# Optimization experiments

Hardware: AMD Instinct MI355X
Metric: run time of the kernel (lower is better)

Reference implementation:

```python
import jax, jax.numpy as jnp
import numpy as np

N_F, N_C = 100000, 25000          # fine / coarse node counts
C_IN, C_OUT = 128, 128
E_POOL, E = 200000, 400000        # pooling edges, coarse point-point edges


def setup_inputs() -> dict:
    key = jax.random.key(0)
    ks = jax.random.split(key, 12)
    x = jax.random.normal(ks[0], (N_F, C_IN), jnp.float32)
    # pooling edges: src in fine graph, dst in coarse graph
    pool_src = jax.random.randint(ks[1], (E_POOL,), 0, N_F, dtype=jnp.int64)
    pool_dst = jax.random.randint(ks[2], (E_POOL,), 0, N_C, dtype=jnp.int64)
    pool_edge_index = jnp.stack([pool_src, pool_dst])
    pool_edge_attr = jax.random.uniform(ks[3], (E_POOL,), jnp.float32)
    # coarse point-point edges
    src = jax.random.randint(ks[4], (E,), 0, N_C, dtype=jnp.int64)
    dst = jax.random.randint(ks[5], (E,), 0, N_C, dtype=jnp.int64)
    edge_index = jnp.stack([src, dst])
    edge_attr = jax.random.uniform(ks[6], (E,), jnp.float32)
    s_in = 1.0 / np.sqrt(C_IN).astype(np.float32)
    s_out = 1.0 / np.sqrt(C_OUT).astype(np.float32)
    W1_root = jax.random.normal(ks[7], (C_IN, C_OUT), jnp.float32) * s_in
    W1_nb = jax.random.normal(ks[8], (C_IN, C_OUT), jnp.float32) * s_in
    b1 = jnp.zeros((C_OUT,), jnp.float32)
    W2_root = jax.random.normal(ks[9], (C_OUT, C_OUT), jnp.float32) * s_out
    W2_nb = jax.random.normal(ks[10], (C_OUT, C_OUT), jnp.float32) * s_out
    b2 = jnp.zeros((C_OUT,), jnp.float32)
    return {
        "x": x,
        "pool_edge_index": pool_edge_index,
        "pool_edge_attr": pool_edge_attr,
        "edge_index": edge_index,
        "edge_attr": edge_attr,
        "W1_root": W1_root, "W1_nb": W1_nb, "b1": b1,
        "W2_root": W2_root, "W2_nb": W2_nb, "b2": b2,
        "n_coarse": N_C,
    }


def _graph_conv(h, edge_index, edge_attr, W_root, W_nb, b, n_nodes):
    # GraphConv with edge weights: out = h @ W_root + scatter_add(w_e * (h[src] @ W_nb), dst) + b
    msg = edge_attr[:, None] * (h[edge_index[0]] @ W_nb)          # [E, C_out]
    agg = jax.ops.segment_sum(msg, edge_index[1], num_segments=n_nodes)
    return h @ W_root + agg + b


def reference(x, pool_edge_index, pool_edge_attr, edge_index, edge_attr,
              W1_root, W1_nb, b1, W2_root, W2_nb, b2, n_coarse):
    # CustomPoolingAdd: weighted scatter-add fine -> coarse
    pooled = jax.ops.segment_sum(pool_edge_attr[:, None] * x[pool_edge_index[0]],
                                 pool_edge_index[1], num_segments=n_coarse)  # [N_c, C_in]
    h = _graph_conv(pooled, edge_index, edge_attr, W1_root, W1_nb, b1, n_coarse)
    h = _graph_conv(h, edge_index, edge_attr, W2_root, W2_nb, b2, n_coarse)
    return h
```

## Files before the change

### kernel.cpp

```cpp
#include <hip/hip_runtime.h>

typedef __attribute__((ext_vector_type(8))) short   short8;
typedef __attribute__((ext_vector_type(8))) __bf16  bf16x8;
typedef __attribute__((ext_vector_type(4))) float   f32x4;

__device__ __forceinline__ float bf2f(unsigned short u) {
    union { unsigned int i; float f; } v; v.i = ((unsigned int)u) << 16; return v.f;
}
__device__ __forceinline__ unsigned short f2bf(float f) {
    union { float f; unsigned int i; } v; v.f = f;
    unsigned int r = v.i + 0x7fffu + ((v.i >> 16) & 1u);
    return (unsigned short)(r >> 16);
}

__device__ __forceinline__ int load_idx(const void* p, int is64, long long i) {
    return is64 ? (int)((const long long*)p)[i] : ((const int*)p)[i];
}
__device__ __forceinline__ float load_f(const void* p, int isbf, long long i) {
    return isbf ? bf2f(((const unsigned short*)p)[i]) : ((const float*)p)[i];
}

__device__ __forceinline__ int self_is64(const int* p) {
    int lane = threadIdx.x & 63;
    unsigned long long b = __ballot(p[2 * lane + 1] != 0);
    return b == 0ull;
}
__device__ __forceinline__ int self_isbf(const unsigned int* p) {
    int lane = threadIdx.x & 63;
    unsigned int lo = p[lane] & 0xFFFFu;
    int e = (int)((lo >> 7) & 0xFF);
    int ok = (lo == 0u) || (e >= 88 && e <= 141);
    return (__ballot(!ok) == 0ull) ? 1 : 0;
}

__global__ void detect_kernel(const int* __restrict__ pei, const int* __restrict__ ei,
                              const unsigned int* f0, const unsigned int* f1,
                              const unsigned int* f2, const unsigned int* f3,
                              const unsigned int* f4, const unsigned int* f5,
                              const unsigned int* f6, const unsigned int* f7,
                              const unsigned int* f8,
                              int* __restrict__ flags) {
    int lane = threadIdx.x & 63;
    unsigned long long ba = __ballot(pei[2 * lane + 1] != 0);
    unsigned long long bb = __ballot(ei[2 * lane + 1] != 0);
    const unsigned int* fa[9] = {f0, f1, f2, f3, f4, f5, f6, f7, f8};
    int bf[9];
    #pragma unroll
    for (int t = 0; t < 9; t++) {
        unsigned int lo = fa[t][lane] & 0xFFFFu;
        int e = (int)((lo >> 7) & 0xFF);
        int ok = (lo == 0u) || (e >= 88 && e <= 141);
        bf[t] = (__ballot(!ok) == 0ull) ? 1 : 0;
    }
    if (lane == 0) {
        flags[0] = (ba == 0ull);
        flags[1] = (bb == 0ull);
        #pragma unroll
        for (int t = 0; t < 9; t++) flags[2 + t] = bf[t];
    }
}

#define BKT_CAP 64
#define OVF_CAP 4096
#define CNT_STRIDE 16

__global__ void fillpack_kernel(const void* __restrict__ pei, const void* __restrict__ pattr,
                                const void* __restrict__ ei, const void* __restrict__ eattr,
                                int* __restrict__ pcnt, int2* __restrict__ pbkt,
                                int* __restrict__ povfc, int4* __restrict__ povf,
                                int* __restrict__ ccnt, int2* __restrict__ cbkt,
                                int* __restrict__ covfc, int4* __restrict__ covf,
                                int Ep, int Ec, int gE,
                                const void* __restrict__ w1r, const void* __restrict__ w1n,
                                const void* __restrict__ w2r, const void* __restrict__ w2n,
                                unsigned short* __restrict__ wpack) {
    if ((int)blockIdx.x >= gE) {
        int gid = ((int)blockIdx.x - gE) * 256 + threadIdx.x;
        int layer = gid >> 15;
        int r = gid & 32767;
        int j = r & 7, lane = (r >> 3) & 63, ch = (r >> 9) & 7, ct = (r >> 12) & 7;
        int n = ct * 16 + (lane & 15);
        int k = ch * 32 + (lane >> 4) * 8 + j;
        const void* w;
        if (layer == 0) w = (k < 128) ? w1r : w1n;
        else            w = (k < 128) ? w2r : w2n;
        int fs = self_isbf((const unsigned int*)w);
        float v = load_f(w, fs, (long long)(k & 127) * 128 + n);
        wpack[gid] = f2bf(v);
        return;
    }
    long long g = (long long)blockIdx.x * 256 + threadIdx.x;
    if (g < Ep) {
        int is64 = self_is64((const int*)pei);
        int abf = self_isbf((const unsigned int*)pattr);
        int s = load_idx(pei, is64, g);
        int d = load_idx(pei, is64, (long long)Ep + g);
        float w = load_f(pattr, abf, g);
        int pos = atomicAdd(&pcnt[d * CNT_STRIDE], 1);
        if (pos < BKT_CAP) {
            pbkt[(long long)d * BKT_CAP + pos] = make_int2(s, __float_as_int(w));
        } else {
            int oi = atomicAdd(povfc, 1);
            if (oi < OVF_CAP) povf[oi] = make_int4(s, __float_as_int(w), d, 0);
        }
    } else if (g - Ep < Ec) {
        long long e = g - Ep;
        int is64 = self_is64((const int*)ei);
        int abf = self_isbf((const unsigned int*)eattr);
        int s = load_idx(ei, is64, e);
        int d = load_idx(ei, is64, (long long)Ec + e);
        float w = load_f(eattr, abf, e);
        int pos = atomicAdd(&ccnt[d * CNT_STRIDE], 1);
        if (pos < BKT_CAP) {
            cbkt[(long long)d * BKT_CAP + pos] = make_int2(s, __float_as_int(w));
        } else {
            int oi = atomicAdd(covfc, 1);
            if (oi < OVF_CAP) covf[oi] = make_int4(s, __float_as_int(w), d, 0);
        }
    }
}

__global__ void gatherb_kernel(const void* __restrict__ in,
                               const int* __restrict__ cnt,
                               const int2* __restrict__ bkt,
                               const int* __restrict__ ovfc,
                               const int4* __restrict__ ovf,
                               unsigned short* __restrict__ out, int NC,
                               int detectIn) {
    int d = blockIdx.x * 4 + (threadIdx.x >> 6);
    if (d >= NC) return;
    int lane = threadIdx.x & 63;
    int j1 = cnt[d * CNT_STRIDE]; if (j1 > BKT_CAP) j1 = BKT_CAP;
    const int2* row = bkt + (long long)d * BKT_CAP;
    float ax = 0.f, ay = 0.f;
    int bf = detectIn ? self_isbf((const unsigned int*)in) : 1;
    if (!bf) {
        const float* fin = (const float*)in;
        int c0 = lane * 2;
        int j = 0;
        for (; j + 8 <= j1; j += 8) {
            int2 e0 = row[j], e1 = row[j + 1], e2 = row[j + 2], e3 = row[j + 3];
            int2 e4 = row[j + 4], e5 = row[j + 5], e6 = row[j + 6], e7 = row[j + 7];
            float2 v0 = *(const float2*)(fin + (long long)e0.x * 128 + c0);
            float2 v1 = *(const float2*)(fin + (long long)e1.x * 128 + c0);
            float2 v2 = *(const float2*)(fin + (long long)e2.x * 128 + c0);
            float2 v3 = *(const float2*)(fin + (long long)e3.x * 128 + c0);
            float2 v4 = *(const float2*)(fin + (long long)e4.x * 128 + c0);
            float2 v5 = *(const float2*)(fin + (long long)e5.x * 128 + c0);
            float2 v6 = *(const float2*)(fin + (long long)e6.x * 128 + c0);
            float2 v7 = *(const float2*)(fin + (long long)e7.x * 128 + c0);
            ax += __int_as_float(e0.y) * v0.x + __int_as_float(e1.y) * v1.x
                + __int_as_float(e2.y) * v2.x + __int_as_float(e3.y) * v3.x
                + __int_as_float(e4.y) * v4.x + __int_as_float(e5.y) * v5.x
                + __int_as_float(e6.y) * v6.x + __int_as_float(e7.y) * v7.x;
            ay += __int_as_float(e0.y) * v0.y + __int_as_float(e1.y) * v1.y
                + __int_as_float(e2.y) * v2.y + __int_as_float(e3.y) * v3.y
                + __int_as_float(e4.y) * v4.y + __int_as_float(e5.y) * v5.y
                + __int_as_float(e6.y) * v6.y + __int_as_float(e7.y) * v7.y;
        }
        for (; j + 4 <= j1; j += 4) {
            int2 e0 = row[j], e1 = row[j + 1], e2 = row[j + 2], e3 = row[j + 3];
            float2 v0 = *(const float2*)(fin + (long long)e0.x * 128 + c0);
            float2 v1 = *(const float2*)(fin + (long long)e1.x * 128 + c0);
            float2 v2 = *(const float2*)(fin + (long long)e2.x * 128 + c0);
            float2 v3 = *(const float2*)(fin + (long long)e3.x * 128 + c0);
            ax += __int_as_float(e0.y) * v0.x + __int_as_float(e1.y) * v1.x
                + __int_as_float(e2.y) * v2.x + __int_as_float(e3.y) * v3.x;
            ay += __int_as_float(e0.y) * v0.y + __int_as_float(e1.y) * v1.y
                + __int_as_float(e2.y) * v2.y + __int_as_float(e3.y) * v3.y;
        }
        for (; j < j1; j++) {
            int2 e = row[j];
            float w = __int_as_float(e.y);
            float2 v = *(const float2*)(fin + (long long)e.x * 128 + c0);
            ax += w * v.x; ay += w * v.y;
        }
        int novf = *ovfc;
        if (novf > 0) {
            if (novf > OVF_CAP) novf = OVF_CAP;
            for (int k = 0; k < novf; k++) {
                int4 e = ovf[k];
                if (e.z == d) {
                    float w = __int_as_float(e.y);
                    float2 v = *(const float2*)(fin + (long long)e.x * 128 + c0);
                    ax += w * v.x; ay += w * v.y;
                }
            }
        }
    } else {
        const unsigned int* uin = (const unsigned int*)in;
        int j = 0;
        for (; j + 8 <= j1; j += 8) {
            int2 e0 = row[j], e1 = row[j + 1], e2 = row[j + 2], e3 = row[j + 3];
            int2 e4 = row[j + 4], e5 = row[j + 5], e6 = row[j + 6], e7 = row[j + 7];
            unsigned int v0 = uin[(long long)e0.x * 64 + lane];
            unsigned int v1 = uin[(long long)e1.x * 64 + lane];
            unsigned int v2 = uin[(long long)e2.x * 64 + lane];
            unsigned int v3 = uin[(long long)e3.x * 64 + lane];
            unsigned int v4 = uin[(long long)e4.x * 64 + lane];
            unsigned int v5 = uin[(long long)e5.x * 64 + lane];
            unsigned int v6 = uin[(long long)e6.x * 64 + lane];
            unsigned int v7 = uin[(long long)e7.x * 64 + lane];
            ax += __int_as_float(e0.y) * bf2f((unsigned short)v0)
                + __int_as_float(e1.y) * bf2f((unsigned short)v1)
                + __int_as_float(e2.y) * bf2f((unsigned short)v2)
                + __int_as_float(e3.y) * bf2f((unsigned short)v3)
                + __int_as_float(e4.y) * bf2f((unsigned short)v4)
                + __int_as_float(e5.y) * bf2f((unsigned short)v5)
                + __int_as_float(e6.y) * bf2f((unsigned short)v6)
                + __int_as_float(e7.y) * bf2f((unsigned short)v7);
            ay += __int_as_float(e0.y) * bf2f((unsigned short)(v0 >> 16))
                + __int_as_float(e1.y) * bf2f((unsigned short)(v1 >> 16))
                + __int_as_float(e2.y) * bf2f((unsigned short)(v2 >> 16))
                + __int_as_float(e3.y) * bf2f((unsigned short)(v3 >> 16))
                + __int_as_float(e4.y) * bf2f((unsigned short)(v4 >> 16))
                + __int_as_float(e5.y) * bf2f((unsigned short)(v5 >> 16))
                + __int_as_float(e6.y) * bf2f((unsigned short)(v6 >> 16))
                + __int_as_float(e7.y) * bf2f((unsigned short)(v7 >> 16));
        }
        for (; j + 4 <= j1; j += 4) {
            int2 e0 = row[j], e1 = row[j + 1], e2 = row[j + 2], e3 = row[j + 3];
            unsigned int v0 = uin[(long long)e0.x * 64 + lane];
            unsigned int v1 = uin[(long long)e1.x * 64 + lane];
            unsigned int v2 = uin[(long long)e2.x * 64 + lane];
            unsigned int v3 = uin[(long long)e3.x * 64 + lane];
            ax += __int_as_float(e0.y) * bf2f((unsigned short)v0)
                + __int_as_float(e1.y) * bf2f((unsigned short)v1)
                + __int_as_float(e2.y) * bf2f((unsigned short)v2)
                + __int_as_float(e3.y) * bf2f((unsigned short)v3);
            ay += __int_as_float(e0.y) * bf2f((unsigned short)(v0 >> 16))
                + __int_as_float(e1.y) * bf2f((unsigned short)(v1 >> 16))
                + __int_as_float(e2.y) * bf2f((unsigned short)(v2 >> 16))
                + __int_as_float(e3.y) * bf2f((unsigned short)(v3 >> 16));
        }
        for (; j < j1; j++) {
            int2 e = row[j];
            float w = __int_as_float(e.y);
            unsigned int v = uin[(long long)e.x * 64 + lane];
            ax += w * bf2f((unsigned short)v);
            ay += w * bf2f((unsigned short)(v >> 16));
        }
        int novf = *ovfc;
        if (novf > 0) {
            if (novf > OVF_CAP) novf = OVF_CAP;
            for (int k = 0; k < novf; k++) {
                int4 e = ovf[k];
                if (e.z == d) {
                    float w = __int_as_float(e.y);
                    unsigned int v = uin[(long long)e.x * 64 + lane];
                    ax += w * bf2f((unsigned short)v);
                    ay += w * bf2f((unsigned short)(v >> 16));
                }
            }
        }
    }
    unsigned int o = (unsigned int)f2bf(ax) | ((unsigned int)f2bf(ay) << 16);
    ((unsigned int*)out)[(long long)d * 64 + lane] = o;
}

__global__ __launch_bounds__(256, 4)
void gemm_mfma_kernel(const unsigned short* __restrict__ H,
                      const unsigned short* __restrict__ G,
                      const unsigned short* __restrict__ wpack,
                      const void* __restrict__ bias,
                      float* __restrict__ outF, unsigned short* __restrict__ outB,
                      int NC) {
    __shared__ unsigned short ldsA[64 * 264];
    int tid = threadIdx.x;
    long long r0 = (long long)blockIdx.x * 64;
    for (int i = tid; i < 4096; i += 256) {
        int mat = i >> 11;
        int flat = i & 2047;
        int row = flat >> 5;
        int c4 = flat & 31;
        long long r = r0 + row;
        const unsigned short* srcp = mat ? G : H;
        uint2 v = make_uint2(0u, 0u);
        if (r < NC) v = *(const uint2*)(srcp + r * 128 + c4 * 4);
        *(uint2*)&ldsA[row * 264 + mat * 128 + c4 * 4] = v;
    }
    __syncthreads();

    int wave = tid >> 6, lane = tid & 63;
    int m = lane & 15, quad = lane >> 4;
    int arow = wave * 16 + m;

    bf16x8 a[8];
    #pragma unroll
    for (int ch = 0; ch < 8; ch++) {
        short8 av = *(const short8*)&ldsA[arow * 264 + ch * 32 + quad * 8];
        a[ch] = __builtin_bit_cast(bf16x8, av);
    }

    f32x4 acc[8];
    #pragma unroll
    for (int ct = 0; ct < 8; ct++) acc[ct] = (f32x4){0.f, 0.f, 0.f, 0.f};

    #pragma unroll
    for (int ct = 0; ct < 8; ct++) {
        #pragma unroll
        for (int ch = 0; ch < 8; ch++) {
            short8 bv = *(const short8*)(wpack + ((ct * 8 + ch) * 64 + lane) * 8);
            acc[ct] = __builtin_amdgcn_mfma_f32_16x16x32_bf16(
                a[ch], __builtin_bit_cast(bf16x8, bv), acc[ct], 0, 0, 0);
        }
    }

    int bbf = self_isbf((const unsigned int*)bias);
    #pragma unroll
    for (int ct = 0; ct < 8; ct++) {
        int n = ct * 16 + m;
        float bv = load_f(bias, bbf, n);
        #pragma unroll
        for (int r = 0; r < 4; r++) {
            long long rr = r0 + wave * 16 + quad * 4 + r;
            if (rr < NC) {
                float val = acc[ct][r] + bv;
                if (outF) outF[rr * 128 + n] = val;
                else      outB[rr * 128 + n] = f2bf(val);
            }
        }
    }
}

__global__ void pool_scatter_kernel(const void* __restrict__ x, const void* __restrict__ pei,
                                    const void* __restrict__ pattr, const int* __restrict__ flags,
                                    float* __restrict__ pooled, int Ep, int CI) {
    int c = blockIdx.y * blockDim.x + threadIdx.x;
    if (c >= CI) return;
    int e = blockIdx.x;
    int is64 = flags[0], xbf = flags[2], abf = flags[3];
    int s = load_idx(pei, is64, e);
    int d = load_idx(pei, is64, (long long)Ep + e);
    float w = load_f(pattr, abf, e);
    float v = load_f(x, xbf, (long long)s * CI + c);
    atomicAdd(&pooled[(long long)d * CI + c], w * v);
}

__global__ void conv_scatter_kernel(const float* __restrict__ t, const void* __restrict__ ei,
                                    const void* __restrict__ attr, const int* __restrict__ flags,
                                    float* __restrict__ outacc, int Ec, int CO) {
    int c = blockIdx.y * blockDim.x + threadIdx.x;
    if (c >= CO) return;
    int e = blockIdx.x;
    int is64 = flags[1], abf = flags[4];
    int s = load_idx(ei, is64, e);
    int d = load_idx(ei, is64, (long long)Ec + e);
    float w = load_f(attr, abf, e);
    atomicAdd(&outacc[(long long)d * CO + c], w * t[(long long)s * CO + c]);
}

__global__ void gemm_kernel(const float* H, const void* __restrict__ Wr,
                            const void* __restrict__ Wn, const void* __restrict__ bias,
                            const int* __restrict__ flags, int fWr, int fWn, int fB,
                            float* out_root, float* out_t, int NC, int CI, int CO) {
    __shared__ float lds[4][1024];
    int wave = threadIdx.x >> 6;
    int lane = threadIdx.x & 63;
    int r = blockIdx.x * 4 + wave;
    if (r < NC) {
        const float* hrow = H + (long long)r * CI;
        for (int k = lane; k < CI; k += 64) lds[wave][k] = hrow[k];
    }
    __syncthreads();
    if (r >= NC) return;
    int wrbf = flags[fWr], wnbf = flags[fWn], bbf = flags[fB];
    for (int c0 = lane * 2; c0 < CO; c0 += 128) {
        int two = (c0 + 1 < CO);
        float ar0 = 0.f, ar1 = 0.f, an0 = 0.f, an1 = 0.f;
        for (int k = 0; k < CI; k++) {
            float h = lds[wave][k];
            ar0 += h * load_f(Wr, wrbf, (long long)k * CO + c0);
            an0 += h * load_f(Wn, wnbf, (long long)k * CO + c0);
            if (two) {
                ar1 += h * load_f(Wr, wrbf, (long long)k * CO + c0 + 1);
                an1 += h * load_f(Wn, wnbf, (long long)k * CO + c0 + 1);
            }
        }
        long long o = (long long)r * CO + c0;
        out_root[o] = ar0 + load_f(bias, bbf, c0);
        out_t[o] = an0;
        if (two) {
            out_root[o + 1] = ar1 + load_f(bias, bbf, c0 + 1);
            out_t[o + 1] = an1;
        }
    }
}

__global__ void to_out_kernel(const float* __restrict__ in, float* __restrict__ out, long long n) {
    long long stride = (long long)gridDim.x * blockDim.x;
    for (long long i = (long long)blockIdx.x * blockDim.x + threadIdx.x; i < n; i += stride)
        out[i] = in[i];
}

extern "C" void kernel_launch(void* const* d_in, const int* in_sizes, int n_in,
                              void* d_out, int out_size, void* d_ws, size_t ws_size,
                              hipStream_t stream) {
    const void* x = d_in[0]; const void* pei = d_in[1]; const void* pattr = d_in[2];
    const void* ei = d_in[3]; const void* eattr = d_in[4];
    const void* w1r = d_in[5]; const void* w1n = d_in[6]; const void* b1 = d_in[7];
    const void* w2r = d_in[8]; const void* w2n = d_in[9]; const void* b2 = d_in[10];

    long long CO = in_sizes[7];
    long long CI = CO > 0 ? in_sizes[5] / CO : 0;
    long long Ep = in_sizes[2];
    long long Ec = in_sizes[4];
    long long NC = CO > 0 ? (long long)out_size / CO : 0;
    int sane = (CO > 0 && CI > 0 && CI <= 1024 && CO <= 1024 &&
                CI * CO == in_sizes[5] && NC * CO == out_size &&
                Ep > 0 && Ec > 0 && in_sizes[0] % CI == 0);
    if (!sane) { CO = 128; CI = 128; Ep = 200000; Ec = 400000; NC = 25000; }

    char* ws = (char*)d_ws;

    if (CI == 128 && CO == 128) {
        size_t off = 0;
        unsigned short* bufP = (unsigned short*)(ws + off); off += (size_t)NC * 128 * 2;
        unsigned short* bufH = (unsigned short*)(ws + off); off += (size_t)NC * 128 * 2;
        unsigned short* bufG = (unsigned short*)(ws + off); off += (size_t)NC * 128 * 2;
        unsigned short* wpack = (unsigned short*)(ws + off); off += 65536 * 2;
        int* pcnt  = (int*)(ws + off); off += NC * CNT_STRIDE * 4;
        int* ccnt  = (int*)(ws + off); off += NC * CNT_STRIDE * 4;
        int* povfc = (int*)(ws + off); off += 4;
        int* covfc = (int*)(ws + off); off += 4;
        off = (off + 15) & ~(size_t)15;
        int4* povf = (int4*)(ws + off); off += (size_t)OVF_CAP * 16;
        int4* covf = (int4*)(ws + off); off += (size_t)OVF_CAP * 16;
        int2* pbkt = (int2*)(ws + off); off += (size_t)NC * BKT_CAP * 8;
        int2* cbkt = (int2*)(ws + off); off += (size_t)NC * BKT_CAP * 8;

        hipMemsetAsync(pcnt, 0, (2 * NC * CNT_STRIDE + 2) * 4, stream);

        int gE = (int)((Ep + Ec + 255) / 256);
        fillpack_kernel<<<gE + 256, 256, 0, stream>>>(pei, pattr, ei, eattr,
                                                      pcnt, pbkt, povfc, povf,
                                                      ccnt, cbkt, covfc, covf,
                                                      (int)Ep, (int)Ec, gE,
                                                      w1r, w1n, w2r, w2n, wpack);

        int gN4 = (int)((NC + 3) / 4);
        int gN64 = (int)((NC + 63) / 64);
        gatherb_kernel<<<gN4, 256, 0, stream>>>(x, pcnt, pbkt, povfc, povf, bufP, (int)NC, 1);
        gatherb_kernel<<<gN4, 256, 0, stream>>>(bufP, ccnt, cbkt, covfc, covf, bufG, (int)NC, 0);
        gemm_mfma_kernel<<<gN64, 256, 0, stream>>>(bufP, bufG, wpack, b1,
                                                   nullptr, bufH, (int)NC);
        gatherb_kernel<<<gN4, 256, 0, stream>>>(bufH, ccnt, cbkt, covfc, covf, bufG, (int)NC, 0);
        gemm_mfma_kernel<<<gN64, 256, 0, stream>>>(bufH, bufG, wpack + 32768, b2,
                                                   (float*)d_out, nullptr, (int)NC);
        return;
    }

    size_t szP = (size_t)NC * CI * sizeof(float);
    size_t szO = (size_t)NC * CO * sizeof(float);
    float *bufP, *bufA, *bufB, *bufC; int* flags;
    if (CI == CO) {
        bufP = (float*)ws; bufA = (float*)(ws + szP);
        bufB = bufP; bufC = bufA;
        flags = (int*)(ws + szP + szO);
    } else {
        bufP = (float*)ws; bufA = (float*)(ws + szP);
        bufB = (float*)(ws + szP + szO); bufC = (float*)(ws + szP + 2 * szO);
        flags = (int*)(ws + szP + 3 * szO);
    }
    detect_kernel<<<1, 64, 0, stream>>>(
        (const int*)pei, (const int*)ei,
        (const unsigned int*)x, (const unsigned int*)pattr, (const unsigned int*)eattr,
        (const unsigned int*)w1r, (const unsigned int*)w1n, (const unsigned int*)b1,
        (const unsigned int*)w2r, (const unsigned int*)w2n, (const unsigned int*)b2,
        flags);
    hipMemsetAsync(bufP, 0, szP, stream);
    int blkP = (CI % 64 == 0 && CI <= 256) ? (int)CI : 256;
    int blkC = (CO % 64 == 0 && CO <= 256) ? (int)CO : 256;
    dim3 gP((unsigned)Ep, (unsigned)((CI + blkP - 1) / blkP));
    dim3 gC((unsigned)Ec, (unsigned)((CO + blkC - 1) / blkC));
    int gG = (int)((NC + 3) / 4);
    pool_scatter_kernel<<<gP, blkP, 0, stream>>>(x, pei, pattr, flags, bufP, (int)Ep, (int)CI);
    if (CI == CO) {
        gemm_kernel<<<gG, 256, 0, stream>>>(bufP, w1r, w1n, b1, flags, 5, 6, 7,
                                            bufA, bufP, (int)NC, (int)CI, (int)CO);
        conv_scatter_kernel<<<gC, blkC, 0, stream>>>(bufP, ei, eattr, flags, bufA, (int)Ec, (int)CO);
        gemm_kernel<<<gG, 256, 0, stream>>>(bufA, w2r, w2n, b2, flags, 8, 9, 10,
                                            bufP, bufA, (int)NC, (int)CO, (int)CO);
        conv_scatter_kernel<<<gC, blkC, 0, stream>>>(bufA, ei, eattr, flags, bufP, (int)Ec, (int)CO);
        to_out_kernel<<<4096, 256, 0, stream>>>(bufP, (float*)d_out, NC * CO);
    } else {
        gemm_kernel<<<gG, 256, 0, stream>>>(bufP, w1r, w1n, b1, flags, 5, 6, 7,
                                            bufA, bufB, (int)NC, (int)CI, (int)CO);
        conv_scatter_kernel<<<gC, blkC, 0, stream>>>(bufB, ei, eattr, flags, bufA, (int)Ec, (int)CO);
        gemm_kernel<<<gG, 256, 0, stream>>>(bufA, w2r, w2n, b2, flags, 8, 9, 10,
                                            bufB, bufC, (int)NC, (int)CO, (int)CO);
        conv_scatter_kernel<<<gC, blkC, 0, stream>>>(bufC, ei, eattr, flags, bufB, (int)Ec, (int)CO);
        to_out_kernel<<<4096, 256, 0, stream>>>(bufB, (float*)d_out, NC * CO);
    }
}
```

Measured before the change: 235.0 us.

## Pre-convert fine features to bf16 and compact bucket counters

Adds extra blocks to the edge-bucketing kernel that convert the fp32 fine-node features x into a bf16 copy in workspace, when the workspace is large enough. The pooling gather then reads half as many bytes per random row through a new gatherx kernel. Per-node counters are packed densely instead of padded to 16 ints, which shrinks the memset, and the pooling bucket capacity drops to 32. The trade-off is an extra streaming pass over x, extra rounding of the input features to bf16, and possibly more atomic contention on the densely packed counters.

```diff
diff --git a/kernel.cpp b/kernel.cpp
--- a/kernel.cpp
+++ b/kernel.cpp
@@ -60,9 +60,9 @@
     }
 }
 
-#define BKT_CAP 64
+#define PBKT_CAP 32
+#define CBKT_CAP 64
 #define OVF_CAP 4096
-#define CNT_STRIDE 16
 
 __global__ void fillpack_kernel(const void* __restrict__ pei, const void* __restrict__ pattr,
                                 const void* __restrict__ ei, const void* __restrict__ eattr,
@@ -73,9 +73,35 @@
                                 int Ep, int Ec, int gE,
                                 const void* __restrict__ w1r, const void* __restrict__ w1n,
                                 const void* __restrict__ w2r, const void* __restrict__ w2n,
-                                unsigned short* __restrict__ wpack) {
-    if ((int)blockIdx.x >= gE) {
-        int gid = ((int)blockIdx.x - gE) * 256 + threadIdx.x;
+                                unsigned short* __restrict__ wpack,
+                                const void* __restrict__ x, unsigned short* __restrict__ xb,
+                                long long elemsX) {
+    int bid = (int)blockIdx.x;
+    if (bid >= gE + 256) {
+        int xisbf = self_isbf((const unsigned int*)x);
+        if (xisbf) return;
+        long long gid = (long long)(bid - gE - 256) * 256 + threadIdx.x;
+        long long row = gid >> 3;
+        int part = (int)(gid & 7);
+        long long NF = elemsX >> 7;
+        if (row >= NF) return;
+        const float4* src = (const float4*)((const float*)x + row * 128 + part * 16);
+        float4 a = src[0], b = src[1], c = src[2], d = src[3];
+        uint4 o0, o1;
+        o0.x = (unsigned int)f2bf(a.x) | ((unsigned int)f2bf(a.y) << 16);
+        o0.y = (unsigned int)f2bf(a.z) | ((unsigned int)f2bf(a.w) << 16);
+        o0.z = (unsigned int)f2bf(b.x) | ((unsigned int)f2bf(b.y) << 16);
+        o0.w = (unsigned int)f2bf(b.z) | ((unsigned int)f2bf(b.w) << 16);
+        o1.x = (unsigned int)f2bf(c.x) | ((unsigned int)f2bf(c.y) << 16);
+        o1.y = (unsigned int)f2bf(c.z) | ((unsigned int)f2bf(c.w) << 16);
+        o1.z = (unsigned int)f2bf(d.x) | ((unsigned int)f2bf(d.y) << 16);
+        o1.w = (unsigned int)f2bf(d.z) | ((unsigned int)f2bf(d.w) << 16);
+        uint4* dst = (uint4*)(xb + row * 128 + part * 16);
+        dst[0] = o0; dst[1] = o1;
+        return;
+    }
+    if (bid >= gE) {
+        int gid = (bid - gE) * 256 + threadIdx.x;
         int layer = gid >> 15;
         int r = gid & 32767;
         int j = r & 7, lane = (r >> 3) & 63, ch = (r >> 9) & 7, ct = (r >> 12) & 7;
@@ -89,16 +115,16 @@
         wpack[gid] = f2bf(v);
         return;
     }
-    long long g = (long long)blockIdx.x * 256 + threadIdx.x;
+    long long g = (long long)bid * 256 + threadIdx.x;
     if (g < Ep) {
         int is64 = self_is64((const int*)pei);
         int abf = self_isbf((const unsigned int*)pattr);
         int s = load_idx(pei, is64, g);
         int d = load_idx(pei, is64, (long long)Ep + g);
         float w = load_f(pattr, abf, g);
-        int pos = atomicAdd(&pcnt[d * CNT_STRIDE], 1);
-        if (pos < BKT_CAP) {
-            pbkt[(long long)d * BKT_CAP + pos] = make_int2(s, __float_as_int(w));
+        int pos = atomicAdd(&pcnt[d], 1);
+        if (pos < PBKT_CAP) {
+            pbkt[(long long)d * PBKT_CAP + pos] = make_int2(s, __float_as_int(w));
         } else {
             int oi = atomicAdd(povfc, 1);
             if (oi < OVF_CAP) povf[oi] = make_int4(s, __float_as_int(w), d, 0);
@@ -110,9 +136,9 @@
         int s = load_idx(ei, is64, e);
         int d = load_idx(ei, is64, (long long)Ec + e);
         float w = load_f(eattr, abf, e);
-        int pos = atomicAdd(&ccnt[d * CNT_STRIDE], 1);
-        if (pos < BKT_CAP) {
-            cbkt[(long long)d * BKT_CAP + pos] = make_int2(s, __float_as_int(w));
+        int pos = atomicAdd(&ccnt[d], 1);
+        if (pos < CBKT_CAP) {
+            cbkt[(long long)d * CBKT_CAP + pos] = make_int2(s, __float_as_int(w));
         } else {
             int oi = atomicAdd(covfc, 1);
             if (oi < OVF_CAP) covf[oi] = make_int4(s, __float_as_int(w), d, 0);
@@ -120,104 +146,23 @@
     }
 }
 
-__global__ void gatherb_kernel(const void* __restrict__ in,
+__global__ void gatherx_kernel(const void* __restrict__ x,
+                               const unsigned short* __restrict__ xb, int haveXb,
                                const int* __restrict__ cnt,
                                const int2* __restrict__ bkt,
                                const int* __restrict__ ovfc,
                                const int4* __restrict__ ovf,
-                               unsigned short* __restrict__ out, int NC,
-                               int detectIn) {
+                               unsigned short* __restrict__ out, int NC) {
     int d = blockIdx.x * 4 + (threadIdx.x >> 6);
     if (d >= NC) return;
     int lane = threadIdx.x & 63;
-    int j1 = cnt[d * CNT_STRIDE]; if (j1 > BKT_CAP) j1 = BKT_CAP;
-    const int2* row = bkt + (long long)d * BKT_CAP;
+    int j1 = cnt[d]; if (j1 > PBKT_CAP) j1 = PBKT_CAP;
+    const int2* row = bkt + (long long)d * PBKT_CAP;
     float ax = 0.f, ay = 0.f;
-    int bf = detectIn ? self_isbf((const unsigned int*)in) : 1;
-    if (!bf) {
-        const float* fin = (const float*)in;
-        int c0 = lane * 2;
+    int xisbf = self_isbf((const unsigned int*)x);
+    if (xisbf || haveXb) {
+        const unsigned int* uin = xisbf ? (const unsigned int*)x : (const unsigned int*)xb;
         int j = 0;
-        for (; j + 8 <= j1; j += 8) {
-            int2 e0 = row[j], e1 = row[j + 1], e2 = row[j + 2], e3 = row[j + 3];
-            int2 e4 = row[j + 4], e5 = row[j + 5], e6 = row[j + 6], e7 = row[j + 7];
-            float2 v0 = *(const float2*)(fin + (long long)e0.x * 128 + c0);
-            float2 v1 = *(const float2*)(fin + (long long)e1.x * 128 + c0);
-            float2 v2 = *(const float2*)(fin + (long long)e2.x * 128 + c0);
-            float2 v3 = *(const float2*)(fin + (long long)e3.x * 128 + c0);
-            float2 v4 = *(const float2*)(fin + (long long)e4.x * 128 + c0);
-            float2 v5 = *(const float2*)(fin + (long long)e5.x * 128 + c0);
-            float2 v6 = *(const float2*)(fin + (long long)e6.x * 128 + c0);
-            float2 v7 = *(const float2*)(fin + (long long)e7.x * 128 + c0);
-            ax += __int_as_float(e0.y) * v0.x + __int_as_float(e1.y) * v1.x
-                + __int_as_float(e2.y) * v2.x + __int_as_float(e3.y) * v3.x
-                + __int_as_float(e4.y) * v4.x + __int_as_float(e5.y) * v5.x
-                + __int_as_float(e6.y) * v6.x + __int_as_float(e7.y) * v7.x;
-            ay += __int_as_float(e0.y) * v0.y + __int_as_float(e1.y) * v1.y
-                + __int_as_float(e2.y) * v2.y + __int_as_float(e3.y) * v3.y
-                + __int_as_float(e4.y) * v4.y + __int_as_float(e5.y) * v5.y
-                + __int_as_float(e6.y) * v6.y + __int_as_float(e7.y) * v7.y;
-        }
-        for (; j + 4 <= j1; j += 4) {
-            int2 e0 = row[j], e1 = row[j + 1], e2 = row[j + 2], e3 = row[j + 3];
-            float2 v0 = *(const float2*)(fin + (long long)e0.x * 128 + c0);
-            float2 v1 = *(const float2*)(fin + (long long)e1.x * 128 + c0);
-            float2 v2 = *(const float2*)(fin + (long long)e2.x * 128 + c0);
-            float2 v3 = *(const float2*)(fin + (long long)e3.x * 128 + c0);
-            ax += __int_as_float(e0.y) * v0.x + __int_as_float(e1.y) * v1.x
-                + __int_as_float(e2.y) * v2.x + __int_as_float(e3.y) * v3.x;
-            ay += __int_as_float(e0.y) * v0.y + __int_as_float(e1.y) * v1.y
-                + __int_as_float(e2.y) * v2.y + __int_as_float(e3.y) * v3.y;
-        }
-        for (; j < j1; j++) {
-            int2 e = row[j];
-            float w = __int_as_float(e.y);
-            float2 v = *(const float2*)(fin + (long long)e.x * 128 + c0);
-            ax += w * v.x; ay += w * v.y;
-        }
-        int novf = *ovfc;
-        if (novf > 0) {
-            if (novf > OVF_CAP) novf = OVF_CAP;
-            for (int k = 0; k < novf; k++) {
-                int4 e = ovf[k];
-                if (e.z == d) {
-                    float w = __int_as_float(e.y);
-                    float2 v = *(const float2*)(fin + (long long)e.x * 128 + c0);
-                    ax += w * v.x; ay += w * v.y;
-                }
-            }
-        }
-    } else {
-        const unsigned int* uin = (const unsigned int*)in;
-        int j = 0;
-        for (; j + 8 <= j1; j += 8) {
-            int2 e0 = row[j], e1 = row[j + 1], e2 = row[j + 2], e3 = row[j + 3];
-            int2 e4 = row[j + 4], e5 = row[j + 5], e6 = row[j + 6], e7 = row[j + 7];
-            unsigned int v0 = uin[(long long)e0.x * 64 + lane];
-            unsigned int v1 = uin[(long long)e1.x * 64 + lane];
-            unsigned int v2 = uin[(long long)e2.x * 64 + lane];
-            unsigned int v3 = uin[(long long)e3.x * 64 + lane];
-            unsigned int v4 = uin[(long long)e4.x * 64 + lane];
-            unsigned int v5 = uin[(long long)e5.x * 64 + lane];
-            unsigned int v6 = uin[(long long)e6.x * 64 + lane];
-            unsigned int v7 = uin[(long long)e7.x * 64 + lane];
-            ax += __int_as_float(e0.y) * bf2f((unsigned short)v0)
-                + __int_as_float(e1.y) * bf2f((unsigned short)v1)
-                + __int_as_float(e2.y) * bf2f((unsigned short)v2)
-                + __int_as_float(e3.y) * bf2f((unsigned short)v3)
-                + __int_as_float(e4.y) * bf2f((unsigned short)v4)
-                + __int_as_float(e5.y) * bf2f((unsigned short)v5)
-                + __int_as_float(e6.y) * bf2f((unsigned short)v6)
-                + __int_as_float(e7.y) * bf2f((unsigned short)v7);
-            ay += __int_as_float(e0.y) * bf2f((unsigned short)(v0 >> 16))
-                + __int_as_float(e1.y) * bf2f((unsigned short)(v1 >> 16))
-                + __int_as_float(e2.y) * bf2f((unsigned short)(v2 >> 16))
-                + __int_as_float(e3.y) * bf2f((unsigned short)(v3 >> 16))
-                + __int_as_float(e4.y) * bf2f((unsigned short)(v4 >> 16))
-                + __int_as_float(e5.y) * bf2f((unsigned short)(v5 >> 16))
-                + __int_as_float(e6.y) * bf2f((unsigned short)(v6 >> 16))
-                + __int_as_float(e7.y) * bf2f((unsigned short)(v7 >> 16));
-        }
         for (; j + 4 <= j1; j += 4) {
             int2 e0 = row[j], e1 = row[j + 1], e2 = row[j + 2], e3 = row[j + 3];
             unsigned int v0 = uin[(long long)e0.x * 64 + lane];
@@ -251,6 +196,120 @@
                     ax += w * bf2f((unsigned short)v);
                     ay += w * bf2f((unsigned short)(v >> 16));
                 }
+            }
+        }
+    } else {
+        const float* fin = (const float*)x;
+        int c0 = lane * 2;
+        int j = 0;
+        for (; j + 4 <= j1; j += 4) {
+            int2 e0 = row[j], e1 = row[j + 1], e2 = row[j + 2], e3 = row[j + 3];
+            float2 v0 = *(const float2*)(fin + (long long)e0.x * 128 + c0);
+            float2 v1 = *(const float2*)(fin + (long long)e1.x * 128 + c0);
+            float2 v2 = *(const float2*)(fin + (long long)e2.x * 128 + c0);
+            float2 v3 = *(const float2*)(fin + (long long)e3.x * 128 + c0);
+            ax += __int_as_float(e0.y) * v0.x + __int_as_float(e1.y) * v1.x
+                + __int_as_float(e2.y) * v2.x + __int_as_float(e3.y) * v3.x;
+            ay += __int_as_float(e0.y) * v0.y + __int_as_float(e1.y) * v1.y
+                + __int_as_float(e2.y) * v2.y + __int_as_float(e3.y) * v3.y;
+        }
+        for (; j < j1; j++) {
+            int2 e = row[j];
+            float w = __int_as_float(e.y);
+            float2 v = *(const float2*)(fin + (long long)e.x * 128 + c0);
+            ax += w * v.x; ay += w * v.y;
+        }
+        int novf = *ovfc;
+        if (novf > 0) {
+            if (novf > OVF_CAP) novf = OVF_CAP;
+            for (int k = 0; k < novf; k++) {
+                int4 e = ovf[k];
+                if (e.z == d) {
+                    float w = __int_as_float(e.y);
+                    float2 v = *(const float2*)(fin + (long long)e.x * 128 + c0);
+                    ax += w * v.x; ay += w * v.y;
+                }
+            }
+        }
+    }
+    unsigned int o = (unsigned int)f2bf(ax) | ((unsigned int)f2bf(ay) << 16);
+    ((unsigned int*)out)[(long long)d * 64 + lane] = o;
+}
+
+__global__ void gatherb_kernel(const unsigned short* __restrict__ in,
+                               const int* __restrict__ cnt,
+                               const int2* __restrict__ bkt, int cap,
+                               const int* __restrict__ ovfc,
+                               const int4* __restrict__ ovf,
+                               unsigned short* __restrict__ out, int NC) {
+    int d = blockIdx.x * 4 + (threadIdx.x >> 6);
+    if (d >= NC) return;
+    int lane = threadIdx.x & 63;
+    int j1 = cnt[d]; if (j1 > cap) j1 = cap;
+    const int2* row = bkt + (long long)d * cap;
+    float ax = 0.f, ay = 0.f;
+    const unsigned int* uin = (const unsigned int*)in;
+    int j = 0;
+    for (; j + 8 <= j1; j += 8) {
+        int2 e0 = row[j], e1 = row[j + 1], e2 = row[j + 2], e3 = row[j + 3];
+        int2 e4 = row[j + 4], e5 = row[j + 5], e6 = row[j + 6], e7 = row[j + 7];
+        unsigned int v0 = uin[(long long)e0.x * 64 + lane];
+        unsigned int v1 = uin[(long long)e1.x * 64 + lane];
+        unsigned int v2 = uin[(long long)e2.x * 64 + lane];
+        unsigned int v3 = uin[(long long)e3.x * 64 + lane];
+        unsigned int v4 = uin[(long long)e4.x * 64 + lane];
+        unsigned int v5 = uin[(long long)e5.x * 64 + lane];
+        unsigned int v6 = uin[(long long)e6.x * 64 + lane];
+        unsigned int v7 = uin[(long long)e7.x * 64 + lane];
+        ax += __int_as_float(e0.y) * bf2f((unsigned short)v0)
+            + __int_as_float(e1.y) * bf2f((unsigned short)v1)
+            + __int_as_float(e2.y) * bf2f((unsigned short)v2)
+            + __int_as_float(e3.y) * bf2f((unsigned short)v3)
+            + __int_as_float(e4.y) * bf2f((unsigned short)v4)
+            + __int_as_float(e5.y) * bf2f((unsigned short)v5)
+            + __int_as_float(e6.y) * bf2f((unsigned short)v6)
+            + __int_as_float(e7.y) * bf2f((unsigned short)v7);
+        ay += __int_as_float(e0.y) * bf2f((unsigned short)(v0 >> 16))
+            + __int_as_float(e1.y) * bf2f((unsigned short)(v1 >> 16))
+            + __int_as_float(e2.y) * bf2f((unsigned short)(v2 >> 16))
+            + __int_as_float(e3.y) * bf2f((unsigned short)(v3 >> 16))
+            + __int_as_float(e4.y) * bf2f((unsigned short)(v4 >> 16))
+            + __int_as_float(e5.y) * bf2f((unsigned short)(v5 >> 16))
+            + __int_as_float(e6.y) * bf2f((unsigned short)(v6 >> 16))
+            + __int_as_float(e7.y) * bf2f((unsigned short)(v7 >> 16));
+    }
+    for (; j + 4 <= j1; j += 4) {
+        int2 e0 = row[j], e1 = row[j + 1], e2 = row[j + 2], e3 = row[j + 3];
+        unsigned int v0 = uin[(long long)e0.x * 64 + lane];
+        unsigned int v1 = uin[(long long)e1.x * 64 + lane];
+        unsigned int v2 = uin[(long long)e2.x * 64 + lane];
+        unsigned int v3 = uin[(long long)e3.x * 64 + lane];
+        ax += __int_as_float(e0.y) * bf2f((unsigned short)v0)
+            + __int_as_float(e1.y) * bf2f((unsigned short)v1)
+            + __int_as_float(e2.y) * bf2f((unsigned short)v2)
+            + __int_as_float(e3.y) * bf2f((unsigned short)v3);
+        ay += __int_as_float(e0.y) * bf2f((unsigned short)(v0 >> 16))
+            + __int_as_float(e1.y) * bf2f((unsigned short)(v1 >> 16))
+            + __int_as_float(e2.y) * bf2f((unsigned short)(v2 >> 16))
+            + __int_as_float(e3.y) * bf2f((unsigned short)(v3 >> 16));
+    }
+    for (; j < j1; j++) {
+        int2 e = row[j];
+        float w = __int_as_float(e.y);
+        unsigned int v = uin[(long long)e.x * 64 + lane];
+        ax += w * bf2f((unsigned short)v);
+        ay += w * bf2f((unsigned short)(v >> 16));
+    }
+    int novf = *ovfc;
+    if (novf > 0) {
+        if (novf > OVF_CAP) novf = OVF_CAP;
+        for (int k = 0; k < novf; k++) {
+            int4 e = ovf[k];
+            if (e.z == d) {
+                float w = __int_as_float(e.y);
+                unsigned int v = uin[(long long)e.x * 64 + lane];
+                ax += w * bf2f((unsigned short)v);
+                ay += w * bf2f((unsigned short)(v >> 16));
             }
         }
     }
@@ -414,37 +473,48 @@
     char* ws = (char*)d_ws;
 
     if (CI == 128 && CO == 128) {
+        long long elemsX = in_sizes[0];
         size_t off = 0;
         unsigned short* bufP = (unsigned short*)(ws + off); off += (size_t)NC * 128 * 2;
         unsigned short* bufH = (unsigned short*)(ws + off); off += (size_t)NC * 128 * 2;
         unsigned short* bufG = (unsigned short*)(ws + off); off += (size_t)NC * 128 * 2;
         unsigned short* wpack = (unsigned short*)(ws + off); off += 65536 * 2;
-        int* pcnt  = (int*)(ws + off); off += NC * CNT_STRIDE * 4;
-        int* ccnt  = (int*)(ws + off); off += NC * CNT_STRIDE * 4;
+        int* pcnt  = (int*)(ws + off); off += NC * 4;
+        int* ccnt  = (int*)(ws + off); off += NC * 4;
         int* povfc = (int*)(ws + off); off += 4;
         int* covfc = (int*)(ws + off); off += 4;
         off = (off + 15) & ~(size_t)15;
         int4* povf = (int4*)(ws + off); off += (size_t)OVF_CAP * 16;
         int4* covf = (int4*)(ws + off); off += (size_t)OVF_CAP * 16;
-        int2* pbkt = (int2*)(ws + off); off += (size_t)NC * BKT_CAP * 8;
-        int2* cbkt = (int2*)(ws + off); off += (size_t)NC * BKT_CAP * 8;
-
-        hipMemsetAsync(pcnt, 0, (2 * NC * CNT_STRIDE + 2) * 4, stream);
+        int2* pbkt = (int2*)(ws + off); off += (size_t)NC * PBKT_CAP * 8;
+        int2* cbkt = (int2*)(ws + off); off += (size_t)NC * CBKT_CAP * 8;
+        off = (off + 15) & ~(size_t)15;
+        unsigned short* xb = (unsigned short*)(ws + off);
+        size_t xbBytes = (size_t)elemsX * 2;
+        int haveXb = (off + xbBytes <= ws_size) ? 1 : 0;
+
+        hipMemsetAsync(pcnt, 0, (2 * NC + 2) * 4, stream);
 
         int gE = (int)((Ep + Ec + 255) / 256);
-        fillpack_kernel<<<gE + 256, 256, 0, stream>>>(pei, pattr, ei, eattr,
-                                                      pcnt, pbkt, povfc, povf,
-                                                      ccnt, cbkt, covfc, covf,
-                                                      (int)Ep, (int)Ec, gE,
-                                                      w1r, w1n, w2r, w2n, wpack);
+        int gConv = haveXb ? (int)((elemsX / 16 + 255) / 256) : 0;
+        fillpack_kernel<<<gE + 256 + gConv, 256, 0, stream>>>(
+            pei, pattr, ei, eattr,
+            pcnt, pbkt, povfc, povf,
+            ccnt, cbkt, covfc, covf,
+            (int)Ep, (int)Ec, gE,
+            w1r, w1n, w2r, w2n, wpack,
+            x, xb, elemsX);
 
         int gN4 = (int)((NC + 3) / 4);
         int gN64 = (int)((NC + 63) / 64);
-        gatherb_kernel<<<gN4, 256, 0, stream>>>(x, pcnt, pbkt, povfc, povf, bufP, (int)NC, 1);
-        gatherb_kernel<<<gN4, 256, 0, stream>>>(bufP, ccnt, cbkt, covfc, covf, bufG, (int)NC, 0);
+        gatherx_kernel<<<gN4, 256, 0, stream>>>(x, xb, haveXb, pcnt, pbkt, povfc, povf,
+                                                bufP, (int)NC);
+        gatherb_kernel<<<gN4, 256, 0, stream>>>(bufP, ccnt, cbkt, CBKT_CAP, covfc, covf,
+                                                bufG, (int)NC);
         gemm_mfma_kernel<<<gN64, 256, 0, stream>>>(bufP, bufG, wpack, b1,
                                                    nullptr, bufH, (int)NC);
-        gatherb_kernel<<<gN4, 256, 0, stream>>>(bufH, ccnt, cbkt, covfc, covf, bufG, (int)NC, 0);
+        gatherb_kernel<<<gN4, 256, 0, stream>>>(bufH, ccnt, cbkt, CBKT_CAP, covfc, covf,
+                                                bufG, (int)NC);
         gemm_mfma_kernel<<<gN64, 256, 0, stream>>>(bufH, bufG, wpack + 32768, b2,
                                                    (float*)d_out, nullptr, (int)NC);
         return;
```

After: 231.8 us. No clear change (-1.3%).
